# Performance work log

Measured on AMD Instinct MI355X. Metric: run time of the kernel, lower is better.

Reference implementation:

```python
import jax, jax.numpy as jnp
import numpy as np

LOC = 200 * 200 + 1   # location vocab
E = 100               # loc_emb_size
H = 100               # hidden_neurons (== input size of STLSTM)
D = 12                # temporal/spatial slot embedding dim
NSLOT = 92


def setup_inputs() -> dict:
    key = jax.random.key(0)
    ks = jax.random.split(key, 24)
    B, T = 1024, 256
    inp = {}
    inp["traj"] = jax.random.randint(ks[0], (B, T), 0, LOC)
    inp["lennew"] = jax.random.randint(ks[1], (B, T), 0, T)
    inp["traj_len"] = 255  # static scalar (loop runs traj_len+1 steps)
    inp["tu"] = jax.random.randint(ks[2], (B, T), 0, NSLOT)
    inp["tl"] = jax.random.randint(ks[3], (B, T), 0, NSLOT)
    inp["tu_slot"] = jax.random.randint(ks[4], (B, T), 0, NSLOT)
    inp["tl_slot"] = jax.random.randint(ks[5], (B, T), 0, NSLOT)
    inp["su"] = jax.random.randint(ks[6], (B, T), 0, NSLOT)
    inp["sl"] = jax.random.randint(ks[7], (B, T), 0, NSLOT)
    inp["su_slot"] = jax.random.randint(ks[8], (B, T), 0, NSLOT)
    inp["sl_slot"] = jax.random.randint(ks[9], (B, T), 0, NSLOT)
    # learned parameters
    inp["emb_loc"] = jax.random.normal(ks[10], (LOC, E), jnp.float32) * 0.02
    inp["emb_t"] = jax.random.normal(ks[11], (NSLOT, D), jnp.float32) * 0.02
    inp["emb_s"] = jax.random.normal(ks[12], (NSLOT, D), jnp.float32) * 0.02
    inp["W_ih"] = jax.random.normal(ks[13], (E, 4 * H), jnp.float32) * 0.05
    inp["W_hh"] = jax.random.normal(ks[14], (H, 4 * H), jnp.float32) * 0.05
    inp["b"] = jnp.zeros((4 * H,), jnp.float32)
    inp["W_xt"] = jax.random.normal(ks[15], (E, H), jnp.float32) * 0.05
    inp["W_tt"] = jax.random.normal(ks[16], (D, H), jnp.float32) * 0.05
    inp["b_t"] = jnp.zeros((H,), jnp.float32)
    inp["W_xs"] = jax.random.normal(ks[17], (E, H), jnp.float32) * 0.05
    inp["W_ss"] = jax.random.normal(ks[18], (D, H), jnp.float32) * 0.05
    inp["b_s"] = jnp.zeros((H,), jnp.float32)
    return inp


def reference(traj, lennew, traj_len, tu, tl, tu_slot, tl_slot, su, sl,
              su_slot, sl_slot, emb_loc, emb_t, emb_s, W_ih, W_hh, b,
              W_xt, W_tt, b_t, W_xs, W_ss, b_s):
    steps = int(traj_len) + 1  # static python int -> static slice
    x = emb_loc[traj[:, :steps]]            # [B, S, E] (dropout is identity in eval)
    dtype = x.dtype

    def interp(up_e, low_e, up_d, low_d):
        # linear interpolation between upper/lower slot embeddings
        up = up_d[:, :steps].astype(dtype)[..., None]
        low = low_d[:, :steps].astype(dtype)[..., None]
        return (up * low_e + low * up_e) / jnp.maximum(up + low, 1.0)

    Tq = interp(emb_t[tu[:, :steps]], emb_t[tl[:, :steps]], tu_slot, tl_slot)  # [B,S,D]
    Sq = interp(emb_s[su[:, :steps]], emb_s[sl[:, :steps]], su_slot, sl_slot)  # [B,S,D]

    B = traj.shape[0]
    h0 = jnp.zeros((B, H), dtype)
    c0 = jnp.zeros((B, H), dtype)
    xs = (x.swapaxes(0, 1), Tq.swapaxes(0, 1), Sq.swapaxes(0, 1))  # time-major

    def step(carry, inp):
        h, c = carry
        xt, tg, sg = inp
        gates = xt @ W_ih + h @ W_hh + b           # [B, 4H]
        i, f, g, o = jnp.split(gates, 4, axis=-1)
        i = jax.nn.sigmoid(i)
        f = jax.nn.sigmoid(f)
        g = jnp.tanh(g)
        o = jax.nn.sigmoid(o)
        tgate = jax.nn.sigmoid(xt @ W_xt + tg @ W_tt + b_t)  # temporal gate
        sgate = jax.nn.sigmoid(xt @ W_xs + sg @ W_ss + b_s)  # spatial gate
        c = f * c + i * tgate * sgate * g
        h = o * jnp.tanh(c)
        return (h, c), None

    (h, c), _ = jax.lax.scan(step, (h0, c0), xs)
    # model returns h at index traj_len, which is the final hidden state
    return h
```

## Files before the change

kernel.cpp:

```cpp
#include <hip/hip_runtime.h>

#define B_    1024
#define T_    256
#define LOCN  40001
#define E_    100
#define H_    100
#define NC    600

constexpr int PROWS = 16;
constexpr int PPAD  = 20;

__global__ __launch_bounds__(320) void proj_loc_kernel(
    const float* __restrict__ emb_loc,
    const float* __restrict__ W_ih,
    const float* __restrict__ W_xt,
    const float* __restrict__ W_xs,
    const float* __restrict__ b,
    const float* __restrict__ b_t,
    const float* __restrict__ b_s,
    float* __restrict__ P)
{
    __shared__ __attribute__((aligned(16))) float aT[E_][PPAD];
    const int tid  = threadIdx.x;
    const int row0 = blockIdx.x * PROWS;

    for (int i = tid; i < PROWS * E_; i += 320) {
        int r = i / E_, k = i - r * E_;
        int rr = row0 + r;
        float v = 0.f;
        if (rr < LOCN) v = emb_loc[rr * E_ + k];
        aT[k][r] = v;
    }
    __syncthreads();
    if (tid >= 300) return;

    for (int cc = 0; cc < 2; ++cc) {
        const int c = tid + cc * 300;
        const float* wp; int stride; float bias;
        if (c < 400)      { wp = W_ih + c;         stride = 400; bias = b[c]; }
        else if (c < 500) { wp = W_xt + (c - 400); stride = 100; bias = b_t[c - 400]; }
        else              { wp = W_xs + (c - 500); stride = 100; bias = b_s[c - 500]; }

        float acc[PROWS];
        #pragma unroll
        for (int r = 0; r < PROWS; ++r) acc[r] = bias;

        for (int k = 0; k < E_; ++k) {
            float w = wp[(size_t)k * stride];
            #pragma unroll
            for (int r = 0; r < PROWS; ++r) acc[r] += aT[k][r] * w;
        }
        #pragma unroll
        for (int r = 0; r < PROWS; ++r) {
            int rr = row0 + r;
            if (rr < LOCN) P[(size_t)rr * NC + c] = acc[r];
        }
    }
}

__global__ void proj_ts_kernel(
    const float* __restrict__ emb_t, const float* __restrict__ emb_s,
    const float* __restrict__ W_tt,  const float* __restrict__ W_ss,
    float* __restrict__ P_t, float* __restrict__ P_s)
{
    int idx = blockIdx.x * 256 + threadIdx.x;
    if (idx >= 2 * 92 * H_) return;
    int which = idx / (92 * H_);
    int rem   = idx - which * (92 * H_);
    int r = rem / H_, c = rem - r * H_;
    const float* e = which ? emb_s : emb_t;
    const float* W = which ? W_ss : W_tt;
    float acc = 0.f;
    #pragma unroll
    for (int k = 0; k < 12; ++k) acc += e[r * 12 + k] * W[k * H_ + c];
    (which ? P_s : P_t)[rem] = acc;
}

constexpr int RB = 4;
constexpr int NT = 704;

__global__ __launch_bounds__(NT, 3) void lstm_rec_kernel(
    const int* __restrict__ traj,
    const int* __restrict__ traj_len_p,
    const int* __restrict__ tu,      const int* __restrict__ tl,
    const int* __restrict__ tu_slot, const int* __restrict__ tl_slot,
    const int* __restrict__ su,      const int* __restrict__ sl,
    const int* __restrict__ su_slot, const int* __restrict__ sl_slot,
    const float* __restrict__ P,
    const float* __restrict__ P_t,
    const float* __restrict__ P_s,
    const float* __restrict__ W_hh,
    float* __restrict__ out)
{
    __shared__ __attribute__((aligned(16))) float h_lds[RB][H_];
    __shared__ float gates_lds[RB][400];
    __shared__ float tg_lds[RB][H_];
    __shared__ float sg_lds[RB][H_];
    __shared__ int   loc_lds[2][RB];

    const int tid = threadIdx.x;
    const int b0  = blockIdx.x * RB;
    int steps = traj_len_p[0] + 1;
    if (steps > T_) steps = T_;

    float w[H_];
    if (tid < 400) {
        #pragma unroll
        for (int k = 0; k < H_; ++k) w[k] = W_hh[k * 400 + tid];
        #pragma unroll
        for (int k = 0; k < H_; ++k) asm volatile("" : "+v"(w[k]));
        ((float*)h_lds)[tid] = 0.f;
    }
    if (tid < RB) loc_lds[0][tid] = traj[(b0 + tid) * T_];

    const int er = tid / 100;
    const int eh = tid - er * 100;
    float c_reg = 0.f, hval = 0.f;
    __syncthreads();

    for (int t = 0; t < steps; ++t) {
        const int buf = t & 1;

        if (tid >= 700) {
            int r = tid - 700;
            if (t + 1 < steps) loc_lds[buf ^ 1][r] = traj[(b0 + r) * T_ + t + 1];
        }

        if (tid < 400) {
            const int n = tid;
            float gacc[RB];
            #pragma unroll
            for (int r = 0; r < RB; ++r)
                gacc[r] = P[(size_t)loc_lds[buf][r] * NC + n];

            float acc[RB] = {0.f, 0.f, 0.f, 0.f};
            #pragma unroll
            for (int k4 = 0; k4 < H_ / 4; ++k4) {
                #pragma unroll
                for (int r = 0; r < RB; ++r) {
                    float4 hv = *(const float4*)(&h_lds[r][k4 * 4]);
                    acc[r] += hv.x * w[k4 * 4 + 0];
                    acc[r] += hv.y * w[k4 * 4 + 1];
                    acc[r] += hv.z * w[k4 * 4 + 2];
                    acc[r] += hv.w * w[k4 * 4 + 3];
                }
            }
            const bool isg = (n >= 200 && n < 300);
            #pragma unroll
            for (int r = 0; r < RB; ++r) {
                float v  = acc[r] + gacc[r];
                float xx = isg ? 2.f * v : v;
                float s  = 1.f / (1.f + expf(-xx));
                gates_lds[r][n] = isg ? (2.f * s - 1.f) : s;
            }
        }

        if (tid >= 448 && tid < 648) {
            const int  ch   = tid - 448;
            const bool is_t = ch < 100;
            const int  hx   = is_t ? ch : ch - 100;
            const int* up_a = is_t ? tu_slot : su_slot;
            const int* lo_a = is_t ? tl_slot : sl_slot;
            const int* ui_a = is_t ? tu : su;
            const int* li_a = is_t ? tl : sl;
            const float* Pq = is_t ? P_t : P_s;
            float* dst      = is_t ? &tg_lds[0][0] : &sg_lds[0][0];
            #pragma unroll
            for (int r = 0; r < RB; ++r) {
                const int off = (b0 + r) * T_ + t;
                float gp  = P[(size_t)loc_lds[buf][r] * NC + 400 + ch];
                float up  = (float)up_a[off];
                float low = (float)lo_a[off];
                int   ui  = ui_a[off], li = li_a[off];
                float iv  = (up * Pq[li * H_ + hx] + low * Pq[ui * H_ + hx])
                            / fmaxf(up + low, 1.f);
                float pre = gp + iv;
                dst[r * H_ + hx] = 1.f / (1.f + expf(-pre));
            }
        }
        __syncthreads();

        if (tid < 400) {
            float i_g = gates_lds[er][eh];
            float f_g = gates_lds[er][100 + eh];
            float g_g = gates_lds[er][200 + eh];
            float o_g = gates_lds[er][300 + eh];
            float tsg = tg_lds[er][eh] * sg_lds[er][eh];
            c_reg = f_g * c_reg + i_g * tsg * g_g;
            hval  = o_g * tanhf(c_reg);
            h_lds[er][eh] = hval;
        }
        __syncthreads();
    }

    if (tid < 400) out[b0 * H_ + tid] = hval;
}

extern "C" void kernel_launch(void* const* d_in, const int* in_sizes, int n_in,
                              void* d_out, int out_size, void* d_ws, size_t ws_size,
                              hipStream_t stream) {
    const int*   traj     = (const int*)  d_in[0];
    const int*   traj_len = (const int*)  d_in[2];
    const int*   tu       = (const int*)  d_in[3];
    const int*   tl       = (const int*)  d_in[4];
    const int*   tu_slot  = (const int*)  d_in[5];
    const int*   tl_slot  = (const int*)  d_in[6];
    const int*   su       = (const int*)  d_in[7];
    const int*   sl       = (const int*)  d_in[8];
    const int*   su_slot  = (const int*)  d_in[9];
    const int*   sl_slot  = (const int*)  d_in[10];
    const float* emb_loc  = (const float*)d_in[11];
    const float* emb_t    = (const float*)d_in[12];
    const float* emb_s    = (const float*)d_in[13];
    const float* W_ih     = (const float*)d_in[14];
    const float* W_hh     = (const float*)d_in[15];
    const float* b        = (const float*)d_in[16];
    const float* W_xt     = (const float*)d_in[17];
    const float* W_tt     = (const float*)d_in[18];
    const float* b_t      = (const float*)d_in[19];
    const float* W_xs     = (const float*)d_in[20];
    const float* W_ss     = (const float*)d_in[21];
    const float* b_s      = (const float*)d_in[22];

    float* P   = (float*)d_ws;
    float* P_t = P + (size_t)LOCN * NC;
    float* P_s = P_t + 92 * H_;

    proj_loc_kernel<<<(LOCN + PROWS - 1) / PROWS, 320, 0, stream>>>(
        emb_loc, W_ih, W_xt, W_xs, b, b_t, b_s, P);
    proj_ts_kernel<<<(2 * 92 * H_ + 255) / 256, 256, 0, stream>>>(
        emb_t, emb_s, W_tt, W_ss, P_t, P_s);
    lstm_rec_kernel<<<B_ / RB, NT, 0, stream>>>(
        traj, traj_len, tu, tl, tu_slot, tl_slot, su, sl, su_slot, sl_slot,
        P, P_t, P_s, W_hh, (float*)d_out);
}
```

Baseline: 832.5 us.

## Stage W_hh in LDS and exchange LSTM gates via lane shuffles

Moves the transposed W_hh (160 KB) from per-thread registers into shared memory. Gate columns are interleaved so each group of four lanes holds i/f/g/o for one hidden unit, and the cell update uses shuffles instead of a gates shared buffer. The t/s gate pair is combined with a shuffle, and the traj prefetch moves into registers. Each thread now keeps four cell states. This lowers register pressure and drops an LDS round trip for the gates, but every step reads the weights from LDS, and the 160 KB allocation likely limits occupancy to one block per CU.

```diff
diff --git a/kernel.cpp b/kernel.cpp
--- a/kernel.cpp
+++ b/kernel.cpp
@@ -79,7 +79,7 @@
 constexpr int RB = 4;
 constexpr int NT = 704;
 
-__global__ __launch_bounds__(NT, 3) void lstm_rec_kernel(
+__global__ __launch_bounds__(NT) void lstm_rec_kernel(
     const int* __restrict__ traj,
     const int* __restrict__ traj_len_p,
     const int* __restrict__ tu,      const int* __restrict__ tl,
@@ -92,108 +92,127 @@
     const float* __restrict__ W_hh,
     float* __restrict__ out)
 {
+    __shared__ __attribute__((aligned(16))) float Wt[400 * H_];
     __shared__ __attribute__((aligned(16))) float h_lds[RB][H_];
-    __shared__ float gates_lds[RB][400];
-    __shared__ float tg_lds[RB][H_];
-    __shared__ float sg_lds[RB][H_];
-    __shared__ int   loc_lds[2][RB];
+    __shared__ __attribute__((aligned(16))) float tsg_lds[RB][H_];
 
     const int tid = threadIdx.x;
     const int b0  = blockIdx.x * RB;
     int steps = traj_len_p[0] + 1;
     if (steps > T_) steps = T_;
-
-    float w[H_];
-    if (tid < 400) {
-        #pragma unroll
-        for (int k = 0; k < H_; ++k) w[k] = W_hh[k * 400 + tid];
-        #pragma unroll
-        for (int k = 0; k < H_; ++k) asm volatile("" : "+v"(w[k]));
-        ((float*)h_lds)[tid] = 0.f;
-    }
-    if (tid < RB) loc_lds[0][tid] = traj[(b0 + tid) * T_];
-
-    const int er = tid / 100;
-    const int eh = tid - er * 100;
-    float c_reg = 0.f, hval = 0.f;
+    steps = __builtin_amdgcn_readfirstlane(steps);
+
+    for (int i = tid; i < E_ * 400; i += NT) {
+        const int k  = i / 400;
+        const int nn = i - k * 400;
+        Wt[nn * H_ + k] = W_hh[i];
+    }
+    if (tid < RB * H_) ((float*)h_lds)[tid] = 0.f;
+
+    const bool isGate = tid < 400;
+    const int  gi = tid & 3;
+    const int  q  = tid >> 2;
+    const int  n  = gi * 100 + q;
+
+    const int  ch   = tid - 448;
+    const bool isTS = (tid >= 448) && (tid < 648);
+    const int  hx   = ch >> 1;
+    const bool lane_t = !(ch & 1);
+    const int* up_a = lane_t ? tu_slot : su_slot;
+    const int* lo_a = lane_t ? tl_slot : sl_slot;
+    const int* ui_a = lane_t ? tu : su;
+    const int* li_a = lane_t ? tl : sl;
+    const float* Pq = lane_t ? P_t : P_s;
+    const int  gcol = (lane_t ? 400 : 500) + hx;
+
+    int tb[RB], lcur[RB], lnxt[RB];
+    #pragma unroll
+    for (int r = 0; r < RB; ++r) {
+        tb[r]   = (b0 + r) * T_;
+        lcur[r] = traj[tb[r]];
+    }
+
+    float c_reg[RB] = {0.f, 0.f, 0.f, 0.f};
     __syncthreads();
 
     for (int t = 0; t < steps; ++t) {
-        const int buf = t & 1;
-
-        if (tid >= 700) {
-            int r = tid - 700;
-            if (t + 1 < steps) loc_lds[buf ^ 1][r] = traj[(b0 + r) * T_ + t + 1];
-        }
-
-        if (tid < 400) {
-            const int n = tid;
+        const int tn = (t + 1 < steps) ? t + 1 : t;
+        float pre[RB];
+
+        if (tid < 648) {
+            #pragma unroll
+            for (int r = 0; r < RB; ++r) lnxt[r] = traj[tb[r] + tn];
+        }
+
+        if (isGate) {
             float gacc[RB];
             #pragma unroll
             for (int r = 0; r < RB; ++r)
-                gacc[r] = P[(size_t)loc_lds[buf][r] * NC + n];
+                gacc[r] = P[(size_t)lcur[r] * NC + n];
 
             float acc[RB] = {0.f, 0.f, 0.f, 0.f};
+            const float* wp = &Wt[n * H_];
             #pragma unroll
             for (int k4 = 0; k4 < H_ / 4; ++k4) {
+                const float4 wv = *(const float4*)(&wp[k4 * 4]);
                 #pragma unroll
                 for (int r = 0; r < RB; ++r) {
-                    float4 hv = *(const float4*)(&h_lds[r][k4 * 4]);
-                    acc[r] += hv.x * w[k4 * 4 + 0];
-                    acc[r] += hv.y * w[k4 * 4 + 1];
-                    acc[r] += hv.z * w[k4 * 4 + 2];
-                    acc[r] += hv.w * w[k4 * 4 + 3];
+                    const float4 hv = *(const float4*)(&h_lds[r][k4 * 4]);
+                    acc[r] += hv.x * wv.x;
+                    acc[r] += hv.y * wv.y;
+                    acc[r] += hv.z * wv.z;
+                    acc[r] += hv.w * wv.w;
                 }
             }
-            const bool isg = (n >= 200 && n < 300);
+            #pragma unroll
+            for (int r = 0; r < RB; ++r) pre[r] = acc[r] + gacc[r];
+        }
+
+        if (isTS) {
             #pragma unroll
             for (int r = 0; r < RB; ++r) {
-                float v  = acc[r] + gacc[r];
-                float xx = isg ? 2.f * v : v;
-                float s  = 1.f / (1.f + expf(-xx));
-                gates_lds[r][n] = isg ? (2.f * s - 1.f) : s;
+                const int off = tb[r] + t;
+                const float gp  = P[(size_t)lcur[r] * NC + gcol];
+                const float up  = (float)up_a[off];
+                const float low = (float)lo_a[off];
+                const int   ui  = ui_a[off], li = li_a[off];
+                const float iv  = (up * Pq[li * H_ + hx] + low * Pq[ui * H_ + hx])
+                                  / fmaxf(up + low, 1.f);
+                const float v   = 1.f / (1.f + expf(-(gp + iv)));
+                const float pv  = __shfl_xor(v, 1);
+                if (lane_t) tsg_lds[r][hx] = v * pv;
             }
         }
-
-        if (tid >= 448 && tid < 648) {
-            const int  ch   = tid - 448;
-            const bool is_t = ch < 100;
-            const int  hx   = is_t ? ch : ch - 100;
-            const int* up_a = is_t ? tu_slot : su_slot;
-            const int* lo_a = is_t ? tl_slot : sl_slot;
-            const int* ui_a = is_t ? tu : su;
-            const int* li_a = is_t ? tl : sl;
-            const float* Pq = is_t ? P_t : P_s;
-            float* dst      = is_t ? &tg_lds[0][0] : &sg_lds[0][0];
+        __syncthreads();
+
+        if (isGate) {
             #pragma unroll
             for (int r = 0; r < RB; ++r) {
-                const int off = (b0 + r) * T_ + t;
-                float gp  = P[(size_t)loc_lds[buf][r] * NC + 400 + ch];
-                float up  = (float)up_a[off];
-                float low = (float)lo_a[off];
-                int   ui  = ui_a[off], li = li_a[off];
-                float iv  = (up * Pq[li * H_ + hx] + low * Pq[ui * H_ + hx])
-                            / fmaxf(up + low, 1.f);
-                float pre = gp + iv;
-                dst[r * H_ + hx] = 1.f / (1.f + expf(-pre));
+                const float v  = pre[r];
+                const bool isg = (gi == 2);
+                const float x  = isg ? 2.f * v : v;
+                const float s  = 1.f / (1.f + expf(-x));
+                const float a  = isg ? 2.f * s - 1.f : s;
+                const float x1 = __shfl_xor(a, 1);
+                const float x2 = __shfl_xor(a, 2);
+                const float x3 = __shfl_xor(x1, 2);
+                if (gi == 0) {
+                    const float tsv = tsg_lds[r][q];
+                    c_reg[r] = x1 * c_reg[r] + a * tsv * x2;
+                    h_lds[r][q] = x3 * tanhf(c_reg[r]);
+                }
             }
         }
+        #pragma unroll
+        for (int r = 0; r < RB; ++r) lcur[r] = lnxt[r];
         __syncthreads();
-
-        if (tid < 400) {
-            float i_g = gates_lds[er][eh];
-            float f_g = gates_lds[er][100 + eh];
-            float g_g = gates_lds[er][200 + eh];
-            float o_g = gates_lds[er][300 + eh];
-            float tsg = tg_lds[er][eh] * sg_lds[er][eh];
-            c_reg = f_g * c_reg + i_g * tsg * g_g;
-            hval  = o_g * tanhf(c_reg);
-            h_lds[er][eh] = hval;
-        }
-        __syncthreads();
-    }
-
-    if (tid < 400) out[b0 * H_ + tid] = hval;
+    }
+
+    if (tid < 400) {
+        const int r  = tid / 100;
+        const int qq = tid - r * 100;
+        out[(b0 + r) * H_ + qq] = h_lds[r][qq];
+    }
 }
 
 extern "C" void kernel_launch(void* const* d_in, const int* in_sizes, int n_in,
```

Result: slower. 1.753 ms (+110.6%).

## Split recurrent matvec K dimension across thread pairs with shuffle reduction

Applied to the files above, without the earlier changes.

The recurrent kernel grows from 704 to 1024 threads. Each of the 400 gate columns is now handled by two threads, each holding 52 of the 100 W_hh rows in registers, and the partial sums are combined with a lane shuffle. The h buffer is padded to 104 columns so the upper half can read it as float4 with zeroed weights. The temporal and spatial gate sigmoids are merged into one thread per hidden unit that writes their product. The goal is to shorten the serial per-step matvec chain and cut register pressure per thread, at the cost of more threads per block and extra shuffle and redundant-sigmoid work.

```diff
diff --git a/kernel.cpp b/kernel.cpp
--- a/kernel.cpp
+++ b/kernel.cpp
@@ -77,9 +77,10 @@
 }
 
 constexpr int RB = 4;
-constexpr int NT = 704;
-
-__global__ __launch_bounds__(NT, 3) void lstm_rec_kernel(
+constexpr int NT = 1024;
+constexpr int HP = 104;
+
+__global__ __launch_bounds__(NT, 4) void lstm_rec_kernel(
     const int* __restrict__ traj,
     const int* __restrict__ traj_len_p,
     const int* __restrict__ tu,      const int* __restrict__ tl,
@@ -92,26 +93,35 @@
     const float* __restrict__ W_hh,
     float* __restrict__ out)
 {
-    __shared__ __attribute__((aligned(16))) float h_lds[RB][H_];
+    __shared__ __attribute__((aligned(16))) float h_lds[RB][HP];
     __shared__ float gates_lds[RB][400];
-    __shared__ float tg_lds[RB][H_];
-    __shared__ float sg_lds[RB][H_];
+    __shared__ float tsg_lds[RB][H_];
     __shared__ int   loc_lds[2][RB];
 
     const int tid = threadIdx.x;
     const int b0  = blockIdx.x * RB;
     int steps = traj_len_p[0] + 1;
     if (steps > T_) steps = T_;
-
-    float w[H_];
-    if (tid < 400) {
-        #pragma unroll
-        for (int k = 0; k < H_; ++k) w[k] = W_hh[k * 400 + tid];
-        #pragma unroll
-        for (int k = 0; k < H_; ++k) asm volatile("" : "+v"(w[k]));
-        ((float*)h_lds)[tid] = 0.f;
-    }
+    steps = __builtin_amdgcn_readfirstlane(steps);
+
+    const bool isGate = tid < 800;
+    const int  half = tid & 1;
+    const int  n    = tid >> 1;
+    const int  kb   = half * 52;
+
+    for (int i = tid; i < RB * HP; i += NT) ((float*)h_lds)[i] = 0.f;
     if (tid < RB) loc_lds[0][tid] = traj[(b0 + tid) * T_];
+
+    float w[52];
+    if (isGate) {
+        #pragma unroll
+        for (int j = 0; j < 52; ++j) {
+            const int k = kb + j;
+            w[j] = (k < 100) ? W_hh[k * 400 + n] : 0.f;
+        }
+        #pragma unroll
+        for (int j = 0; j < 52; ++j) asm volatile("" : "+v"(w[j]));
+    }
 
     const int er = tid / 100;
     const int eh = tid - er * 100;
@@ -121,71 +131,81 @@
     for (int t = 0; t < steps; ++t) {
         const int buf = t & 1;
 
-        if (tid >= 700) {
-            int r = tid - 700;
+        if (tid >= 960 && tid < 964) {
+            const int r = tid - 960;
             if (t + 1 < steps) loc_lds[buf ^ 1][r] = traj[(b0 + r) * T_ + t + 1];
         }
 
-        if (tid < 400) {
-            const int n = tid;
-            float gacc[RB];
-            #pragma unroll
-            for (int r = 0; r < RB; ++r)
-                gacc[r] = P[(size_t)loc_lds[buf][r] * NC + n];
-
-            float acc[RB] = {0.f, 0.f, 0.f, 0.f};
-            #pragma unroll
-            for (int k4 = 0; k4 < H_ / 4; ++k4) {
+        if (isGate) {
+            float gacc[RB] = {0.f, 0.f, 0.f, 0.f};
+            if (half == 0) {
+                #pragma unroll
+                for (int r = 0; r < RB; ++r)
+                    gacc[r] = P[(size_t)loc_lds[buf][r] * NC + n];
+            }
+            float acc[RB];
+            #pragma unroll
+            for (int r = 0; r < RB; ++r) acc[r] = gacc[r];
+            #pragma unroll
+            for (int j4 = 0; j4 < 13; ++j4) {
                 #pragma unroll
                 for (int r = 0; r < RB; ++r) {
-                    float4 hv = *(const float4*)(&h_lds[r][k4 * 4]);
-                    acc[r] += hv.x * w[k4 * 4 + 0];
-                    acc[r] += hv.y * w[k4 * 4 + 1];
-                    acc[r] += hv.z * w[k4 * 4 + 2];
-                    acc[r] += hv.w * w[k4 * 4 + 3];
+                    const float4 hv = *(const float4*)(&h_lds[r][kb + j4 * 4]);
+                    acc[r] += hv.x * w[j4 * 4 + 0];
+                    acc[r] += hv.y * w[j4 * 4 + 1];
+                    acc[r] += hv.z * w[j4 * 4 + 2];
+                    acc[r] += hv.w * w[j4 * 4 + 3];
                 }
             }
-            const bool isg = (n >= 200 && n < 300);
-            #pragma unroll
-            for (int r = 0; r < RB; ++r) {
-                float v  = acc[r] + gacc[r];
-                float xx = isg ? 2.f * v : v;
-                float s  = 1.f / (1.f + expf(-xx));
-                gates_lds[r][n] = isg ? (2.f * s - 1.f) : s;
-            }
-        }
-
-        if (tid >= 448 && tid < 648) {
-            const int  ch   = tid - 448;
-            const bool is_t = ch < 100;
-            const int  hx   = is_t ? ch : ch - 100;
-            const int* up_a = is_t ? tu_slot : su_slot;
-            const int* lo_a = is_t ? tl_slot : sl_slot;
-            const int* ui_a = is_t ? tu : su;
-            const int* li_a = is_t ? tl : sl;
-            const float* Pq = is_t ? P_t : P_s;
-            float* dst      = is_t ? &tg_lds[0][0] : &sg_lds[0][0];
+            const float v0 = acc[0] + __shfl_xor(acc[0], 1);
+            const float v1 = acc[1] + __shfl_xor(acc[1], 1);
+            const float v2 = acc[2] + __shfl_xor(acc[2], 1);
+            const float v3 = acc[3] + __shfl_xor(acc[3], 1);
+            const bool  isg = (n >= 200 && n < 300);
+            const float va  = half ? v2 : v0;
+            const float vb  = half ? v3 : v1;
+            const float xa  = isg ? 2.f * va : va;
+            const float xb  = isg ? 2.f * vb : vb;
+            const float sa  = 1.f / (1.f + expf(-xa));
+            const float sb  = 1.f / (1.f + expf(-xb));
+            const float aa  = isg ? (2.f * sa - 1.f) : sa;
+            const float ab  = isg ? (2.f * sb - 1.f) : sb;
+            const int   rA  = half * 2;
+            gates_lds[rA][n]     = aa;
+            gates_lds[rA + 1][n] = ab;
+        }
+
+        if (tid >= 832 && tid < 932) {
+            const int hx = tid - 832;
             #pragma unroll
             for (int r = 0; r < RB; ++r) {
                 const int off = (b0 + r) * T_ + t;
-                float gp  = P[(size_t)loc_lds[buf][r] * NC + 400 + ch];
-                float up  = (float)up_a[off];
-                float low = (float)lo_a[off];
-                int   ui  = ui_a[off], li = li_a[off];
-                float iv  = (up * Pq[li * H_ + hx] + low * Pq[ui * H_ + hx])
-                            / fmaxf(up + low, 1.f);
-                float pre = gp + iv;
-                dst[r * H_ + hx] = 1.f / (1.f + expf(-pre));
+                const int loc = loc_lds[buf][r];
+                const float gpt = P[(size_t)loc * NC + 400 + hx];
+                const float upt = (float)tu_slot[off];
+                const float lot = (float)tl_slot[off];
+                const int   uit = tu[off], lit = tl[off];
+                const float ivt = (upt * P_t[lit * H_ + hx] + lot * P_t[uit * H_ + hx])
+                                  / fmaxf(upt + lot, 1.f);
+                const float tv  = 1.f / (1.f + expf(-(gpt + ivt)));
+                const float gps = P[(size_t)loc * NC + 500 + hx];
+                const float ups = (float)su_slot[off];
+                const float los = (float)sl_slot[off];
+                const int   uis = su[off], lis = sl[off];
+                const float ivs = (ups * P_s[lis * H_ + hx] + los * P_s[uis * H_ + hx])
+                                  / fmaxf(ups + los, 1.f);
+                const float sv  = 1.f / (1.f + expf(-(gps + ivs)));
+                tsg_lds[r][hx] = tv * sv;
             }
         }
         __syncthreads();
 
         if (tid < 400) {
-            float i_g = gates_lds[er][eh];
-            float f_g = gates_lds[er][100 + eh];
-            float g_g = gates_lds[er][200 + eh];
-            float o_g = gates_lds[er][300 + eh];
-            float tsg = tg_lds[er][eh] * sg_lds[er][eh];
+            const float i_g = gates_lds[er][eh];
+            const float f_g = gates_lds[er][100 + eh];
+            const float g_g = gates_lds[er][200 + eh];
+            const float o_g = gates_lds[er][300 + eh];
+            const float tsg = tsg_lds[er][eh];
             c_reg = f_g * c_reg + i_g * tsg * g_g;
             hval  = o_g * tanhf(c_reg);
             h_lds[er][eh] = hval;
```

Result: slower. 897.1 us (+7.8%).
